# Performance work log

Hardware: AMD Instinct MI355X
Metric: run time of the kernel (lower is better)

## Reference

```python
import jax, jax.numpy as jnp
import numpy as np

FEAT_DIM = 512
NUM_CLASS = 100000
N = 512
M = 0.5
S = 64.0
COS_M = float(np.cos(M))
SIN_M = float(np.sin(M))
THRESHOLD = float(np.cos(np.pi - M))
MM = float(np.sin(np.pi - M) * M)
LABEL_SMOOTH = 0.1


def setup_inputs() -> dict:
    key = jax.random.key(0)
    k1, k2, k3 = jax.random.split(key, 3)
    embbedings = jax.random.normal(k1, (N, FEAT_DIM), dtype=jnp.float32)
    label = jax.random.randint(k2, (N,), 0, NUM_CLASS, dtype=jnp.int64 if jax.config.jax_enable_x64 else jnp.int32)
    w = 0.01 * jax.random.normal(k3, (FEAT_DIM, NUM_CLASS), dtype=jnp.float32)
    return {"embbedings": embbedings, "w": w, "label": label}


def reference(embbedings, w, label):
    n = embbedings.shape[0]
    rows = jnp.arange(n)

    # weight column-normalize (done with no_grad in torch) and feature row-normalize
    wn = w / jnp.linalg.norm(w, axis=0, keepdims=True)
    e = embbedings / jnp.linalg.norm(embbedings, axis=1, keepdims=True)

    cos_theta = jnp.clip(e @ wn, -1.0, 1.0)          # [N, C]
    target_logit = cos_theta[rows, label][:, None]    # [N, 1]

    sin_theta = jnp.sqrt(1.0 - target_logit ** 2)
    cos_theta_m = target_logit * COS_M - sin_theta * SIN_M  # cos(theta + m)

    mask = cos_theta > cos_theta_m                    # hard examples
    final_target_logit = jnp.where(target_logit > THRESHOLD,
                                   cos_theta_m, target_logit - MM)

    # adaptive t (running buffer starts at 0 -> single-step value), no grad in torch
    t = jax.lax.stop_gradient(0.01 * jnp.mean(target_logit))

    cos_theta = jnp.where(mask, cos_theta * (t + cos_theta), cos_theta)
    cos_theta = cos_theta.at[rows, label].set(final_target_logit[:, 0])

    logits = cos_theta * S
    logp = jax.nn.log_softmax(logits, axis=-1)
    nll = -logp[rows, label]
    smooth = -jnp.mean(logp, axis=-1)  # eps/C * sum_c(-logp) == eps * mean(-logp)
    loss = jnp.mean((1.0 - LABEL_SMOOTH) * nll + LABEL_SMOOTH * smooth)
    return loss
```

## Files before the change

kernel.cpp:

```cpp
#include <hip/hip_runtime.h>

#define KD    512
#define NCLS  100000
#define BC    64
#define NB    ((NCLS + BC - 1) / BC)
#define NTILE 1564
#define CPAD  100096
#define R1B   64
#define R1C   25
#define S_SCALE 64.0f
#define COS_M   0.87758256189037276f
#define SIN_M   0.47942553860420301f
#define THRESH (-0.87758256189037276f)
#define MM_C    0.23971276930210151f

typedef __attribute__((ext_vector_type(8))) short short8;
typedef __attribute__((ext_vector_type(4))) float f32x4;

union Pack8 { unsigned short u[8]; uint4 v; };

__device__ __forceinline__ unsigned short f2bf(float x) {
  unsigned int u = __float_as_uint(x);
  u += 0x7fffu + ((u >> 16) & 1u);
  return (unsigned short)(u >> 16);
}

__global__ void k0_norm_target(const float* __restrict__ emb, const float* __restrict__ w,
                               const int* __restrict__ label,
                               unsigned short* __restrict__ eb, float* __restrict__ tlA) {
  int r = blockIdx.x;
  int l = threadIdx.x;
  const float* src = emb + (size_t)r * KD + l * 8;
  float v[8];
  float ss = 0.f;
#pragma unroll
  for (int j = 0; j < 8; ++j) { v[j] = src[j]; ss += v[j] * v[j]; }
#pragma unroll
  for (int m = 1; m < 64; m <<= 1) ss += __shfl_xor(ss, m, 64);
  float rn = rsqrtf(ss);
  Pack8 p;
#pragma unroll
  for (int j = 0; j < 8; ++j) {
    float x = v[j] * rn;
    v[j] = x;
    p.u[j] = f2bf(x);
  }
  *reinterpret_cast<uint4*>(eb + (size_t)r * KD + l * 8) = p.v;

  int lab = label[r];
  float wv[8];
#pragma unroll
  for (int j = 0; j < 8; ++j) wv[j] = w[(size_t)(l * 8 + j) * NCLS + lab];
  float dot = 0.f, sq = 0.f;
#pragma unroll
  for (int j = 0; j < 8; ++j) { dot += v[j] * wv[j]; sq += wv[j] * wv[j]; }
#pragma unroll
  for (int m = 1; m < 64; m <<= 1) {
    dot += __shfl_xor(dot, m, 64);
    sq  += __shfl_xor(sq, m, 64);
  }
  if (l == 0) {
    float tl = dot * rsqrtf(sq);
    tlA[r] = fminf(1.f, fmaxf(-1.f, tl));
  }
}

__global__ void k_prep(const float* __restrict__ tlA, float* __restrict__ ctmA,
                       float* __restrict__ finA, float* __restrict__ tval) {
  __shared__ float red[512];
  int i = threadIdx.x;
  float tl = tlA[i];
  red[i] = tl;
  __syncthreads();
  for (int s = 256; s > 0; s >>= 1) {
    if (i < s) red[i] += red[i + s];
    __syncthreads();
  }
  float st = sqrtf(fmaxf(0.f, 1.f - tl * tl));
  float ctm = tl * COS_M - st * SIN_M;
  ctmA[i] = ctm;
  finA[i] = (tl > THRESH) ? ctm : (tl - MM_C);
  if (i == 0) tval[0] = 0.01f * red[0] * (1.f / 512.f);
}

__global__ __launch_bounds__(256)
void k_w(const float* __restrict__ w, unsigned short* __restrict__ wb,
         float* __restrict__ sqpart) {
  const int tid = threadIdx.x;
  const int ch  = blockIdx.x >> 2;
  const int kh  = blockIdx.x & 3;
  const int c   = ch * 256 + tid;
  const int cc  = (c < NCLS) ? c : (NCLS - 1);
  const bool valid = (c < NCLS);
  const int cb = c >> 6;
  const int ct = (c >> 4) & 3;
  const int cl = c & 15;
  unsigned short* gdst = wb + (size_t)cb * 32768 + ct * 128 + cl * 8;
  const float* srcc = w + cc;
  float sq = 0.f;
#pragma unroll 2
  for (int o16 = 0; o16 < 16; ++o16) {
    const int o = kh * 16 + o16;
    float v[8];
#pragma unroll
    for (int j = 0; j < 8; ++j)
      v[j] = srcc[(size_t)(o * 8 + j) * NCLS];
    Pack8 p;
#pragma unroll
    for (int j = 0; j < 8; ++j) {
      float x = valid ? v[j] : 0.f;
      sq += x * x;
      p.u[j] = f2bf(x);
    }
    *reinterpret_cast<uint4*>(gdst + (size_t)o * 512) = p.v;
  }
  sqpart[(size_t)kh * CPAD + c] = sq;
}

__global__ __launch_bounds__(256, 2)
void k_gemm(const unsigned short* __restrict__ wb, const float* __restrict__ sqpart,
            const unsigned short* __restrict__ eb,
            const int* __restrict__ label, const float* __restrict__ ctmA,
            const float* __restrict__ finA, const float* __restrict__ tval,
            float2* __restrict__ part) {
  __shared__ float invnS[BC];
  __shared__ float sE[512];
  __shared__ float sL[512];
  const int tid = threadIdx.x;
  const int wv = tid >> 6;
  const int l  = tid & 63;
  const int c0 = blockIdx.x * BC;

  if (tid < BC) {
    const int c = c0 + tid;
    float s = sqpart[0 * (size_t)CPAD + c] + sqpart[1 * (size_t)CPAD + c]
            + sqpart[2 * (size_t)CPAD + c] + sqpart[3 * (size_t)CPAD + c];
    invnS[tid] = (s > 0.f) ? rsqrtf(s) : 0.f;
  }
  __syncthreads();

  const int q  = l >> 4;
  const int cl = l & 15;
  const int rbase = wv * 128;
  const unsigned short* bt = wb + (size_t)blockIdx.x * 32768 + q * 512 + cl * 8;
  f32x4 acc[8][4] = {};

#pragma unroll 1
  for (int s = 0; s < 16; ++s) {
    const int k0 = s * 32 + q * 8;
    short8 a[8], b[4];
#pragma unroll
    for (int ct = 0; ct < 4; ++ct)
      b[ct] = *reinterpret_cast<const short8*>(bt + s * 2048 + ct * 128);
#pragma unroll
    for (int rt = 0; rt < 8; ++rt) {
      int row = rbase + rt * 16 + cl;
      a[rt] = *reinterpret_cast<const short8*>(eb + (size_t)row * KD + k0);
    }
#pragma unroll
    for (int rt = 0; rt < 8; ++rt)
#pragma unroll
      for (int ct = 0; ct < 4; ++ct)
        acc[rt][ct] = __builtin_amdgcn_mfma_f32_16x16x32_bf16(a[rt], b[ct], acc[rt][ct], 0, 0, 0);
  }

  const float t = tval[0];
#pragma unroll
  for (int rt = 0; rt < 8; ++rt) {
#pragma unroll
    for (int rg = 0; rg < 4; ++rg) {
      const int row = rbase + rt * 16 + q * 4 + rg;
      const float ctm = ctmA[row];
      const float fin = finA[row];
      const int   lab = label[row];
      float se = 0.f, sl = 0.f;
#pragma unroll
      for (int ct = 0; ct < 4; ++ct) {
        const int cg = c0 + ct * 16 + cl;
        if (cg < NCLS) {
          float cosv = acc[rt][ct][rg] * invnS[ct * 16 + cl];
          cosv = fminf(1.f, fmaxf(-1.f, cosv));
          float logit = (cosv > ctm) ? cosv * (t + cosv) : cosv;
          if (cg == lab) logit = fin;
          float x = S_SCALE * logit;
          se += __expf(x);
          sl += x;
        }
      }
#pragma unroll
      for (int m = 1; m < 16; m <<= 1) {
        se += __shfl_xor(se, m, 64);
        sl += __shfl_xor(sl, m, 64);
      }
      if (cl == 0) { sE[row] = se; sL[row] = sl; }
    }
  }
  __syncthreads();

  {
    float2* dst = part + (size_t)blockIdx.x * 512;
    dst[tid]       = make_float2(sE[tid],       sL[tid]);
    dst[tid + 256] = make_float2(sE[tid + 256], sL[tid + 256]);
  }
}

__global__ __launch_bounds__(256, 2)
void k_gemm_legacy(const float* __restrict__ w, const unsigned short* __restrict__ eb,
            const int* __restrict__ label, const float* __restrict__ ctmA,
            const float* __restrict__ finA, const float* __restrict__ tval,
            float2* __restrict__ part) {
  __shared__ __align__(16) unsigned short Bs[BC * KD];
  __shared__ float ssW[4][BC];
  __shared__ float invnS[BC];
  __shared__ float sE[512];
  __shared__ float sL[512];
  const int tid = threadIdx.x;
  const int wv = tid >> 6;
  const int l  = tid & 63;
  const int c0 = blockIdx.x * BC;
  {
    const int c = l;
    const int cgc = (c0 + c < NCLS) ? (c0 + c) : (NCLS - 1);
    const float* wp = w + cgc;
    float ss = 0.f;
#pragma unroll 1
    for (int ph = 0; ph < 2; ++ph) {
      float vb[8][8];
#pragma unroll
      for (int b = 0; b < 8; ++b) {
        const int kb = wv * 8 + (ph * 8 + b) * 32;
#pragma unroll
        for (int j = 0; j < 8; ++j)
          vb[b][j] = __builtin_nontemporal_load(&wp[(size_t)(kb + j) * NCLS]);
      }
      __builtin_amdgcn_sched_barrier(0);
#pragma unroll
      for (int b = 0; b < 8; ++b) {
        const int kb = wv * 8 + (ph * 8 + b) * 32;
        Pack8 p;
#pragma unroll
        for (int j = 0; j < 8; ++j) {
          float x = vb[b][j];
          ss += x * x;
          p.u[j] = f2bf(x);
        }
        const int G = c * 64 + ((kb >> 3) ^ (c & 7));
        *reinterpret_cast<uint4*>(&Bs[G * 8]) = p.v;
      }
    }
    ssW[wv][c] = ss;
  }
  __syncthreads();
  if (tid < BC) {
    float s = ssW[0][tid] + ssW[1][tid] + ssW[2][tid] + ssW[3][tid];
    invnS[tid] = (s > 0.f) ? rsqrtf(s) : 0.f;
  }
  __syncthreads();
  const int q  = l >> 4;
  const int cl = l & 15;
  const int rbase = wv * 128;
  f32x4 acc[8][4] = {};
#pragma unroll 1
  for (int s = 0; s < 16; ++s) {
    const int k0 = s * 32 + q * 8;
    short8 a[8], b[4];
#pragma unroll
    for (int ct = 0; ct < 4; ++ct) {
      int c = ct * 16 + cl;
      int G = c * 64 + ((k0 >> 3) ^ (c & 7));
      b[ct] = *reinterpret_cast<const short8*>(&Bs[G * 8]);
    }
#pragma unroll
    for (int rt = 0; rt < 8; ++rt) {
      int row = rbase + rt * 16 + cl;
      a[rt] = *reinterpret_cast<const short8*>(eb + (size_t)row * KD + k0);
    }
#pragma unroll
    for (int rt = 0; rt < 8; ++rt)
#pragma unroll
      for (int ct = 0; ct < 4; ++ct)
        acc[rt][ct] = __builtin_amdgcn_mfma_f32_16x16x32_bf16(a[rt], b[ct], acc[rt][ct], 0, 0, 0);
  }
  const float t = tval[0];
#pragma unroll
  for (int rt = 0; rt < 8; ++rt) {
#pragma unroll
    for (int rg = 0; rg < 4; ++rg) {
      const int row = rbase + rt * 16 + q * 4 + rg;
      const float ctm = ctmA[row];
      const float fin = finA[row];
      const int   lab = label[row];
      float se = 0.f, sl = 0.f;
#pragma unroll
      for (int ct = 0; ct < 4; ++ct) {
        const int cg = c0 + ct * 16 + cl;
        if (cg < NCLS) {
          float cosv = acc[rt][ct][rg] * invnS[ct * 16 + cl];
          cosv = fminf(1.f, fmaxf(-1.f, cosv));
          float logit = (cosv > ctm) ? cosv * (t + cosv) : cosv;
          if (cg == lab) logit = fin;
          float x = S_SCALE * logit;
          se += __expf(x);
          sl += x;
        }
      }
#pragma unroll
      for (int m = 1; m < 16; m <<= 1) {
        se += __shfl_xor(se, m, 64);
        sl += __shfl_xor(sl, m, 64);
      }
      if (cl == 0) { sE[row] = se; sL[row] = sl; }
    }
  }
  __syncthreads();
  {
    float2* dst = part + (size_t)blockIdx.x * 512;
    dst[tid]       = make_float2(sE[tid],       sL[tid]);
    dst[tid + 256] = make_float2(sE[tid + 256], sL[tid + 256]);
  }
}

__global__ void k_reduce1(const float2* __restrict__ part, float2* __restrict__ part2) {
  const int j = blockIdx.x;
  const int r = threadIdx.x;
  const int i0 = j * R1C;
  const int i1 = (i0 + R1C < NB) ? (i0 + R1C) : NB;
  float se = 0.f, sl = 0.f;
  for (int i = i0; i < i1; ++i) {
    float2 p = part[(size_t)i * 512 + r];
    se += p.x; sl += p.y;
  }
  part2[(size_t)j * 512 + r] = make_float2(se, sl);
}

__global__ void k_loss(const float2* __restrict__ part2, const float* __restrict__ finA,
                       float* __restrict__ out) {
  __shared__ float red[512];
  const int r = threadIdx.x;
  float se = 0.f, sl = 0.f;
#pragma unroll 4
  for (int j = 0; j < R1B; ++j) {
    float2 p = part2[(size_t)j * 512 + r];
    se += p.x; sl += p.y;
  }
  float lse = logf(se);
  float nll = lse - S_SCALE * finA[r];
  float sm  = lse - sl * (1.f / (float)NCLS);
  red[r] = 0.9f * nll + 0.1f * sm;
  __syncthreads();
  for (int s = 256; s > 0; s >>= 1) {
    if (r < s) red[r] += red[r + s];
    __syncthreads();
  }
  if (r == 0) out[0] = red[0] * (1.f / 512.f);
}

extern "C" void kernel_launch(void* const* d_in, const int* in_sizes, int n_in,
                              void* d_out, int out_size, void* d_ws, size_t ws_size,
                              hipStream_t stream) {
  (void)in_sizes; (void)n_in; (void)out_size;
  const float* emb = (const float*)d_in[0];
  const float* w   = (const float*)d_in[1];
  const int*   lab = (const int*)d_in[2];
  float* out = (float*)d_out;

  char* ws = (char*)d_ws;
  unsigned short* eb = (unsigned short*)ws;
  float* tlA   = (float*)(ws + 524288);
  float* ctmA  = tlA  + 512;
  float* finA  = ctmA + 512;
  float* tval  = finA + 512;
  float2* part  = (float2*)(ws + 524288 + 8192);
  float2* part2 = part + (size_t)NB * 512;
  const size_t wb_off = 7196672;
  unsigned short* wb = (unsigned short*)(ws + wb_off);
  float* sqpart = (float*)(ws + wb_off + (size_t)NTILE * 65536);
  const size_t need = wb_off + (size_t)NTILE * 65536 + (size_t)4 * CPAD * 4;

  if (ws_size >= need) {
    hipLaunchKernelGGL(k_w,  dim3(1564), dim3(256), 0, stream, w, wb, sqpart);
    hipLaunchKernelGGL(k0_norm_target, dim3(512), dim3(64), 0, stream, emb, w, lab, eb, tlA);
    hipLaunchKernelGGL(k_prep, dim3(1), dim3(512), 0, stream, tlA, ctmA, finA, tval);
    hipLaunchKernelGGL(k_gemm, dim3(NB), dim3(256), 0, stream,
                       wb, sqpart, eb, lab, ctmA, finA, tval, part);
  } else {
    hipLaunchKernelGGL(k0_norm_target, dim3(512), dim3(64), 0, stream, emb, w, lab, eb, tlA);
    hipLaunchKernelGGL(k_prep, dim3(1), dim3(512), 0, stream, tlA, ctmA, finA, tval);
    hipLaunchKernelGGL(k_gemm_legacy, dim3(NB), dim3(256), 0, stream,
                       w, eb, lab, ctmA, finA, tval, part);
  }
  hipLaunchKernelGGL(k_reduce1, dim3(R1B), dim3(512), 0, stream, part, part2);
  hipLaunchKernelGGL(k_loss,    dim3(1),   dim3(512), 0, stream, part2, finA, out);
}
```

Measured before the change: 489.9 us.

## Split target-logit gather into parallel kernel and widen GEMM and weight-convert blocks

The target-logit computation is split out of the embedding normalization into a separate kernel, k_tgt. Each of its 64 blocks handles an 8-wide K slice across all 512 rows, and k_prep2 reduces the partials, so the strided label-column gather of w is spread across more threads. The weight-conversion kernel now uses 1024-thread blocks with nontemporal loads and guards writes past CPAD. The GEMM runs 512 threads with 8 waves of 64 rows each, halving accumulators per wave to raise occupancy. The trade-off is an extra launch and partial buffer, while each wave reloads the B fragments for fewer rows.

```diff
diff --git a/kernel.cpp b/kernel.cpp
--- a/kernel.cpp
+++ b/kernel.cpp
@@ -25,9 +25,8 @@
   return (unsigned short)(u >> 16);
 }
 
-__global__ void k0_norm_target(const float* __restrict__ emb, const float* __restrict__ w,
-                               const int* __restrict__ label,
-                               unsigned short* __restrict__ eb, float* __restrict__ tlA) {
+__global__ void k0_norm(const float* __restrict__ emb,
+                        unsigned short* __restrict__ eb, float* __restrict__ rnA) {
   int r = blockIdx.x;
   int l = threadIdx.x;
   const float* src = emb + (size_t)r * KD + l * 8;
@@ -40,58 +39,66 @@
   float rn = rsqrtf(ss);
   Pack8 p;
 #pragma unroll
-  for (int j = 0; j < 8; ++j) {
-    float x = v[j] * rn;
-    v[j] = x;
-    p.u[j] = f2bf(x);
-  }
+  for (int j = 0; j < 8; ++j) p.u[j] = f2bf(v[j] * rn);
   *reinterpret_cast<uint4*>(eb + (size_t)r * KD + l * 8) = p.v;
-
-  int lab = label[r];
-  float wv[8];
-#pragma unroll
-  for (int j = 0; j < 8; ++j) wv[j] = w[(size_t)(l * 8 + j) * NCLS + lab];
+  if (l == 0) rnA[r] = rn;
+}
+
+__global__ __launch_bounds__(512)
+void k_tgt(const float* __restrict__ emb, const float* __restrict__ w,
+           const int* __restrict__ label, float2* __restrict__ tpart) {
+  const int j = blockIdx.x;
+  const int r = threadIdx.x;
+  const int lab = label[r];
+  const float* wc = w + lab;
+  const float* er = emb + (size_t)r * KD + j * 8;
   float dot = 0.f, sq = 0.f;
 #pragma unroll
-  for (int j = 0; j < 8; ++j) { dot += v[j] * wv[j]; sq += wv[j] * wv[j]; }
-#pragma unroll
-  for (int m = 1; m < 64; m <<= 1) {
-    dot += __shfl_xor(dot, m, 64);
-    sq  += __shfl_xor(sq, m, 64);
-  }
-  if (l == 0) {
-    float tl = dot * rsqrtf(sq);
-    tlA[r] = fminf(1.f, fmaxf(-1.f, tl));
-  }
-}
-
-__global__ void k_prep(const float* __restrict__ tlA, float* __restrict__ ctmA,
-                       float* __restrict__ finA, float* __restrict__ tval) {
+  for (int kk = 0; kk < 8; ++kk) {
+    float wv = wc[(size_t)(j * 8 + kk) * NCLS];
+    float ev = er[kk];
+    dot += ev * wv;
+    sq  += wv * wv;
+  }
+  tpart[(size_t)j * 512 + r] = make_float2(dot, sq);
+}
+
+__global__ void k_prep2(const float2* __restrict__ tpart, const float* __restrict__ rnA,
+                        float* __restrict__ ctmA, float* __restrict__ finA,
+                        float* __restrict__ tval) {
   __shared__ float red[512];
-  int i = threadIdx.x;
-  float tl = tlA[i];
-  red[i] = tl;
+  const int r = threadIdx.x;
+  float dot = 0.f, sq = 0.f;
+#pragma unroll 8
+  for (int j = 0; j < 64; ++j) {
+    float2 p = tpart[(size_t)j * 512 + r];
+    dot += p.x; sq += p.y;
+  }
+  float tl = dot * rnA[r] * rsqrtf(sq);
+  tl = fminf(1.f, fmaxf(-1.f, tl));
+  red[r] = tl;
   __syncthreads();
   for (int s = 256; s > 0; s >>= 1) {
-    if (i < s) red[i] += red[i + s];
+    if (r < s) red[r] += red[r + s];
     __syncthreads();
   }
   float st = sqrtf(fmaxf(0.f, 1.f - tl * tl));
   float ctm = tl * COS_M - st * SIN_M;
-  ctmA[i] = ctm;
-  finA[i] = (tl > THRESH) ? ctm : (tl - MM_C);
-  if (i == 0) tval[0] = 0.01f * red[0] * (1.f / 512.f);
-}
-
-__global__ __launch_bounds__(256)
+  ctmA[r] = ctm;
+  finA[r] = (tl > THRESH) ? ctm : (tl - MM_C);
+  if (r == 0) tval[0] = 0.01f * red[0] * (1.f / 512.f);
+}
+
+__global__ __launch_bounds__(1024)
 void k_w(const float* __restrict__ w, unsigned short* __restrict__ wb,
          float* __restrict__ sqpart) {
   const int tid = threadIdx.x;
   const int ch  = blockIdx.x >> 2;
   const int kh  = blockIdx.x & 3;
-  const int c   = ch * 256 + tid;
+  const int c   = ch * 1024 + tid;
   const int cc  = (c < NCLS) ? c : (NCLS - 1);
   const bool valid = (c < NCLS);
+  const bool wvalid = (c < CPAD);
   const int cb = c >> 6;
   const int ct = (c >> 4) & 3;
   const int cl = c & 15;
@@ -104,7 +111,7 @@
     float v[8];
 #pragma unroll
     for (int j = 0; j < 8; ++j)
-      v[j] = srcc[(size_t)(o * 8 + j) * NCLS];
+      v[j] = __builtin_nontemporal_load(&srcc[(size_t)(o * 8 + j) * NCLS]);
     Pack8 p;
 #pragma unroll
     for (int j = 0; j < 8; ++j) {
@@ -112,12 +119,12 @@
       sq += x * x;
       p.u[j] = f2bf(x);
     }
-    *reinterpret_cast<uint4*>(gdst + (size_t)o * 512) = p.v;
-  }
-  sqpart[(size_t)kh * CPAD + c] = sq;
-}
-
-__global__ __launch_bounds__(256, 2)
+    if (wvalid) *reinterpret_cast<uint4*>(gdst + (size_t)o * 512) = p.v;
+  }
+  if (wvalid) sqpart[(size_t)kh * CPAD + c] = sq;
+}
+
+__global__ __launch_bounds__(512, 4)
 void k_gemm(const unsigned short* __restrict__ wb, const float* __restrict__ sqpart,
             const unsigned short* __restrict__ eb,
             const int* __restrict__ label, const float* __restrict__ ctmA,
@@ -141,24 +148,24 @@
 
   const int q  = l >> 4;
   const int cl = l & 15;
-  const int rbase = wv * 128;
+  const int rbase = wv * 64;
   const unsigned short* bt = wb + (size_t)blockIdx.x * 32768 + q * 512 + cl * 8;
-  f32x4 acc[8][4] = {};
+  f32x4 acc[4][4] = {};
 
 #pragma unroll 1
   for (int s = 0; s < 16; ++s) {
     const int k0 = s * 32 + q * 8;
-    short8 a[8], b[4];
+    short8 a[4], b[4];
 #pragma unroll
     for (int ct = 0; ct < 4; ++ct)
       b[ct] = *reinterpret_cast<const short8*>(bt + s * 2048 + ct * 128);
 #pragma unroll
-    for (int rt = 0; rt < 8; ++rt) {
+    for (int rt = 0; rt < 4; ++rt) {
       int row = rbase + rt * 16 + cl;
       a[rt] = *reinterpret_cast<const short8*>(eb + (size_t)row * KD + k0);
     }
 #pragma unroll
-    for (int rt = 0; rt < 8; ++rt)
+    for (int rt = 0; rt < 4; ++rt)
 #pragma unroll
       for (int ct = 0; ct < 4; ++ct)
         acc[rt][ct] = __builtin_amdgcn_mfma_f32_16x16x32_bf16(a[rt], b[ct], acc[rt][ct], 0, 0, 0);
@@ -166,7 +173,7 @@
 
   const float t = tval[0];
 #pragma unroll
-  for (int rt = 0; rt < 8; ++rt) {
+  for (int rt = 0; rt < 4; ++rt) {
 #pragma unroll
     for (int rg = 0; rg < 4; ++rg) {
       const int row = rbase + rt * 16 + q * 4 + rg;
@@ -197,11 +204,64 @@
   }
   __syncthreads();
 
-  {
-    float2* dst = part + (size_t)blockIdx.x * 512;
-    dst[tid]       = make_float2(sE[tid],       sL[tid]);
-    dst[tid + 256] = make_float2(sE[tid + 256], sL[tid + 256]);
-  }
+  part[(size_t)blockIdx.x * 512 + tid] = make_float2(sE[tid], sL[tid]);
+}
+
+__global__ void k0_norm_target_legacy(const float* __restrict__ emb, const float* __restrict__ w,
+                               const int* __restrict__ label,
+                               unsigned short* __restrict__ eb, float* __restrict__ tlA) {
+  int r = blockIdx.x;
+  int l = threadIdx.x;
+  const float* src = emb + (size_t)r * KD + l * 8;
+  float v[8];
+  float ss = 0.f;
+#pragma unroll
+  for (int j = 0; j < 8; ++j) { v[j] = src[j]; ss += v[j] * v[j]; }
+#pragma unroll
+  for (int m = 1; m < 64; m <<= 1) ss += __shfl_xor(ss, m, 64);
+  float rn = rsqrtf(ss);
+  Pack8 p;
+#pragma unroll
+  for (int j = 0; j < 8; ++j) {
+    float x = v[j] * rn;
+    v[j] = x;
+    p.u[j] = f2bf(x);
+  }
+  *reinterpret_cast<uint4*>(eb + (size_t)r * KD + l * 8) = p.v;
+  int lab = label[r];
+  float wv[8];
+#pragma unroll
+  for (int j = 0; j < 8; ++j) wv[j] = w[(size_t)(l * 8 + j) * NCLS + lab];
+  float dot = 0.f, sq = 0.f;
+#pragma unroll
+  for (int j = 0; j < 8; ++j) { dot += v[j] * wv[j]; sq += wv[j] * wv[j]; }
+#pragma unroll
+  for (int m = 1; m < 64; m <<= 1) {
+    dot += __shfl_xor(dot, m, 64);
+    sq  += __shfl_xor(sq, m, 64);
+  }
+  if (l == 0) {
+    float tl = dot * rsqrtf(sq);
+    tlA[r] = fminf(1.f, fmaxf(-1.f, tl));
+  }
+}
+
+__global__ void k_prep(const float* __restrict__ tlA, float* __restrict__ ctmA,
+                       float* __restrict__ finA, float* __restrict__ tval) {
+  __shared__ float red[512];
+  int i = threadIdx.x;
+  float tl = tlA[i];
+  red[i] = tl;
+  __syncthreads();
+  for (int s = 256; s > 0; s >>= 1) {
+    if (i < s) red[i] += red[i + s];
+    __syncthreads();
+  }
+  float st = sqrtf(fmaxf(0.f, 1.f - tl * tl));
+  float ctm = tl * COS_M - st * SIN_M;
+  ctmA[i] = ctm;
+  finA[i] = (tl > THRESH) ? ctm : (tl - MM_C);
+  if (i == 0) tval[0] = 0.01f * red[0] * (1.f / 512.f);
 }
 
 __global__ __launch_bounds__(256, 2)
@@ -376,15 +436,18 @@
   unsigned short* wb = (unsigned short*)(ws + wb_off);
   float* sqpart = (float*)(ws + wb_off + (size_t)NTILE * 65536);
   const size_t need = wb_off + (size_t)NTILE * 65536 + (size_t)4 * CPAD * 4;
+  float*  rnA   = (float*)part;
+  float2* tpart = (float2*)((char*)part + 2048);
 
   if (ws_size >= need) {
-    hipLaunchKernelGGL(k_w,  dim3(1564), dim3(256), 0, stream, w, wb, sqpart);
-    hipLaunchKernelGGL(k0_norm_target, dim3(512), dim3(64), 0, stream, emb, w, lab, eb, tlA);
-    hipLaunchKernelGGL(k_prep, dim3(1), dim3(512), 0, stream, tlA, ctmA, finA, tval);
-    hipLaunchKernelGGL(k_gemm, dim3(NB), dim3(256), 0, stream,
+    hipLaunchKernelGGL(k_w,     dim3(392), dim3(1024), 0, stream, w, wb, sqpart);
+    hipLaunchKernelGGL(k0_norm, dim3(512), dim3(64),   0, stream, emb, eb, rnA);
+    hipLaunchKernelGGL(k_tgt,   dim3(64),  dim3(512),  0, stream, emb, w, lab, tpart);
+    hipLaunchKernelGGL(k_prep2, dim3(1),   dim3(512),  0, stream, tpart, rnA, ctmA, finA, tval);
+    hipLaunchKernelGGL(k_gemm,  dim3(NB),  dim3(512),  0, stream,
                        wb, sqpart, eb, lab, ctmA, finA, tval, part);
   } else {
-    hipLaunchKernelGGL(k0_norm_target, dim3(512), dim3(64), 0, stream, emb, w, lab, eb, tlA);
+    hipLaunchKernelGGL(k0_norm_target_legacy, dim3(512), dim3(64), 0, stream, emb, w, lab, eb, tlA);
     hipLaunchKernelGGL(k_prep, dim3(1), dim3(512), 0, stream, tlA, ctmA, finA, tval);
     hipLaunchKernelGGL(k_gemm_legacy, dim3(NB), dim3(256), 0, stream,
                        w, eb, lab, ctmA, finA, tval, part);
```

Result: faster. 469.2 us (-4.2%).
